# Kernel optimization log

Measured on AMD Instinct MI355X. Metric: run time of the kernel, lower is better.

## Reference

```python
import jax, jax.numpy as jnp
import numpy as np


def _spmm(rows, cols, vals, h, n):
    # sparse_dense_matmul(A, h) with A in COO form: out[r] += val * h[c]
    return jax.ops.segment_sum(vals[:, None] * h[cols], rows, num_segments=n)


def setup_inputs() -> dict:
    key = jax.random.key(0)
    ks = jax.random.split(key, 8)
    N, Din, Dout, D, E = 50000, 256, 128, 8, 800000
    x = jax.random.normal(ks[0], (N, Din), jnp.float32)
    h = jax.random.normal(ks[1], (N, Dout), jnp.float32)
    rows = jax.random.randint(ks[2], (D, E), 0, N, dtype=jnp.int32)
    cols = jax.random.randint(ks[3], (D, E), 0, N, dtype=jnp.int32)
    vals = jax.random.uniform(ks[4], (D, E), jnp.float32)
    W = jax.random.normal(ks[5], (Din, Dout), jnp.float32) * 0.05
    V = jax.random.normal(ks[6], (Dout, Dout), jnp.float32) * 0.05
    alpha = jax.random.normal(ks[7], (D, 1), jnp.float32)
    return dict(x=x, h=h, rows=rows, cols=cols, vals=vals, W=W, V=V, alpha=alpha)


def reference(x, h, rows, cols, vals, W, V, alpha):
    N = x.shape[0]
    D = rows.shape[0]
    # h1 = x @ W (x is tf.SparseTensor in the original; same math densely)
    h1 = x @ W
    # per-device: (A_d @ h) @ V  -> [D, N, Dout]; loop over small fixed device set
    h2 = jnp.stack([_spmm(rows[d], cols[d], vals[d], h, N) @ V for d in range(D)])
    # tf.nn.softmax on [D,1] normalizes the size-1 last axis -> all ones (faithful)
    w = jax.nn.softmax(alpha, axis=-1)[:, 0]  # [D]
    comb = jnp.einsum('dno,d->no', h2, w)  # matches reshape/transpose/matmul combine
    return jax.nn.relu(h1 + comb)
```

## Files before the change

kernel.cpp:

```cpp
#include <hip/hip_runtime.h>
#include <hip/hip_bf16.h>

#define DOUT 128
#define DIN  256
#define BROWS 64
#define MAXNB 1024
#define BIN_CHUNK 4096
#define SCHUNK 9216

typedef __attribute__((ext_vector_type(8))) short bf16x8;
typedef __attribute__((ext_vector_type(4))) float f32x4;
union FragU { uint4 q; bf16x8 f; };

static __device__ __forceinline__ float bf16lo_to_f(unsigned u) {
    return __uint_as_float(u << 16);
}
static __device__ __forceinline__ float bf16hi_to_f(unsigned u) {
    return __uint_as_float(u & 0xffff0000u);
}
static __device__ __forceinline__ unsigned f_to_bf16_bits(float f) {
    unsigned u = __float_as_uint(f);
    return (u + 0x7fffu + ((u >> 16) & 1u)) >> 16;
}
static __device__ __forceinline__ unsigned pack2(float a, float b) {
    return f_to_bf16_bits(a) | (f_to_bf16_bits(b) << 16);
}

__global__ __launch_bounds__(256) void conv_wv(const float* __restrict__ W,
                                               const float* __restrict__ V,
                                               unsigned short* __restrict__ WT,
                                               unsigned short* __restrict__ VT) {
    int n = blockIdx.x;
    int t = threadIdx.x;
    WT[n * 256 + t] = (unsigned short)f_to_bf16_bits(W[t * DOUT + n]);
    if (t < 128) VT[n * 128 + t] = (unsigned short)f_to_bf16_bits(V[t * DOUT + n]);
}

__global__ __launch_bounds__(256) void hv_gemm(const float* __restrict__ h,
                                               const unsigned* __restrict__ VTu,
                                               unsigned short* __restrict__ hV,
                                               int N) {
    __shared__ unsigned xs[64 * 20];
    int t = threadIdx.x;
    int r0 = blockIdx.x * 64;
    int w = t >> 6, l = t & 63;
    int wm = w >> 1, wn = w & 1;
    int lm = l & 15, lk = l >> 4;
    f32x4 acc[2][4];
#pragma unroll
    for (int i = 0; i < 2; ++i)
#pragma unroll
        for (int j = 0; j < 4; ++j) acc[i][j] = (f32x4){0.f, 0.f, 0.f, 0.f};

    int srow = min(r0 + (t >> 2), N - 1);
    const float* hrow = h + (size_t)srow * DOUT + (t & 3) * 8;
    unsigned* xsw = &xs[(t >> 2) * 20 + (t & 3) * 4];

    for (int k0 = 0; k0 < DOUT; k0 += 32) {
        float4 f0 = *(const float4*)(hrow + k0);
        float4 f1 = *(const float4*)(hrow + k0 + 4);
        ((uint4*)xsw)[0] = make_uint4(pack2(f0.x, f0.y), pack2(f0.z, f0.w),
                                      pack2(f1.x, f1.y), pack2(f1.z, f1.w));
        __syncthreads();
        FragU a[2], b[4];
#pragma unroll
        for (int i = 0; i < 2; ++i)
            a[i].q = *(const uint4*)&xs[(wm * 32 + i * 16 + lm) * 20 + lk * 4];
#pragma unroll
        for (int j = 0; j < 4; ++j)
            b[j].q = *(const uint4*)(VTu + (size_t)(wn * 64 + j * 16 + lm) * 64 +
                                     (k0 >> 1) + lk * 4);
#pragma unroll
        for (int i = 0; i < 2; ++i)
#pragma unroll
            for (int j = 0; j < 4; ++j)
                acc[i][j] = __builtin_amdgcn_mfma_f32_16x16x32_bf16(
                    a[i].f, b[j].f, acc[i][j], 0, 0, 0);
        __syncthreads();
    }
#pragma unroll
    for (int i = 0; i < 2; ++i)
#pragma unroll
        for (int j = 0; j < 4; ++j) {
            int gr0 = r0 + wm * 32 + i * 16 + lk * 4;
            int gc = wn * 64 + j * 16 + lm;
#pragma unroll
            for (int r = 0; r < 4; ++r) {
                int gr = gr0 + r;
                if (gr < N)
                    hV[(size_t)gr * DOUT + gc] =
                        (unsigned short)f_to_bf16_bits(acc[i][j][r]);
            }
        }
}

__global__ void bucket_hist(const int* __restrict__ rows, int* __restrict__ gcnt,
                            int nE, int nb) {
    __shared__ int hc[MAXNB];
    for (int i = threadIdx.x; i < nb; i += blockDim.x) hc[i] = 0;
    __syncthreads();
    for (int i = blockIdx.x * blockDim.x + threadIdx.x; i < nE;
         i += gridDim.x * blockDim.x)
        atomicAdd(&hc[rows[i] / BROWS], 1);
    __syncthreads();
    for (int i = threadIdx.x; i < nb; i += blockDim.x)
        if (hc[i]) atomicAdd(&gcnt[i], hc[i]);
}

__global__ __launch_bounds__(1024) void scan_buckets(const int* __restrict__ gcnt,
                                                     int* __restrict__ bptr,
                                                     int* __restrict__ gcur, int nb) {
    __shared__ int wtot[16];
    int t = threadIdx.x;
    int c = (t < nb) ? gcnt[t] : 0;
    int v = c;
#pragma unroll
    for (int d = 1; d < 64; d <<= 1) {
        int u = __shfl_up(v, d);
        if ((t & 63) >= d) v += u;
    }
    if ((t & 63) == 63) wtot[t >> 6] = v;
    __syncthreads();
    if (t < 16) {
        int wv = wtot[t];
#pragma unroll
        for (int d = 1; d < 16; d <<= 1) {
            int u = __shfl_up(wv, d);
            if (t >= d) wv += u;
        }
        wtot[t] = wv;
    }
    __syncthreads();
    int incl = v + ((t >= 64) ? wtot[(t >> 6) - 1] : 0);
    if (t == 0) bptr[0] = 0;
    if (t < nb) { bptr[t + 1] = incl; gcur[t] = incl - c; }
}

__global__ __launch_bounds__(1024) void bin_edges(const int* __restrict__ rows,
                                                  const int* __restrict__ cols,
                                                  const float* __restrict__ vals,
                                                  int* __restrict__ gcur,
                                                  unsigned* __restrict__ ecv4,
                                                  unsigned char* __restrict__ erow,
                                                  int nE, int nb) {
    __shared__ unsigned secv[BIN_CHUNK];
    __shared__ unsigned short srow16[BIN_CHUNK];
    __shared__ int hcnt[MAXNB], loff[MAXNB], lcur[MAXNB], gbase[MAXNB];
    __shared__ int wtot[16];
    int t = threadIdx.x;
    int base = blockIdx.x * BIN_CHUNK;
    int nvalid = min(BIN_CHUNK, nE - base);
    hcnt[t] = 0;
    __syncthreads();
    for (int j = t; j < nvalid; j += 1024)
        atomicAdd(&hcnt[rows[base + j] / BROWS], 1);
    __syncthreads();
    int myc = hcnt[t];
    int v = myc;
#pragma unroll
    for (int d = 1; d < 64; d <<= 1) {
        int u = __shfl_up(v, d);
        if ((t & 63) >= d) v += u;
    }
    if ((t & 63) == 63) wtot[t >> 6] = v;
    __syncthreads();
    if (t < 16) {
        int wv = wtot[t];
#pragma unroll
        for (int d = 1; d < 16; d <<= 1) {
            int u = __shfl_up(wv, d);
            if (t >= d) wv += u;
        }
        wtot[t] = wv;
    }
    __syncthreads();
    int excl = v - myc + ((t >= 64) ? wtot[(t >> 6) - 1] : 0);
    loff[t] = excl;
    lcur[t] = excl;
    if (t < nb && myc > 0) gbase[t] = atomicAdd(&gcur[t], myc);
    __syncthreads();
    for (int j = t; j < nvalid; j += 1024) {
        int i = base + j;
        unsigned r = (unsigned)rows[i];
        int bk = (int)r / BROWS;
        int slot = atomicAdd(&lcur[bk], 1);
        secv[slot] = ((unsigned)cols[i] << 16) | f_to_bf16_bits(vals[i]);
        srow16[slot] = (unsigned short)r;
    }
    __syncthreads();
    for (int j = t; j < nvalid; j += 1024) {
        unsigned r = srow16[j];
        int bk = (int)r / BROWS;
        int dst = gbase[bk] + (j - loff[bk]);
        ecv4[dst] = secv[j];
        erow[dst] = (unsigned char)(r & (BROWS - 1));
    }
}

__global__ __launch_bounds__(512) void spmm_epi(const int* __restrict__ bptr,
                                                const unsigned* __restrict__ ecv4,
                                                const unsigned char* __restrict__ erow,
                                                const unsigned* __restrict__ hV,
                                                const float* __restrict__ x,
                                                const unsigned* __restrict__ WTu,
                                                float* __restrict__ out, int N) {
    __shared__ __align__(16) unsigned srec[SCHUNK + BROWS * 8];
    __shared__ int rcnt[BROWS], rptr[BROWS + 1], rcur[BROWS];
    int t = threadIdx.x;
    int b = blockIdx.x;
    int wave = t >> 6, lane = t & 63;
    int hf = lane >> 5;
    int cl = lane & 31;
    int beg = bptr[b], end = bptr[b + 1];
    const uint2* hv2 = (const uint2*)hV;

    float4 acc[8];
#pragma unroll
    for (int j = 0; j < 8; ++j) acc[j] = make_float4(0.f, 0.f, 0.f, 0.f);

    for (int cb = beg; cb < end; cb += SCHUNK) {
        int nval = min(SCHUNK, end - cb);
        if (t < BROWS) rcnt[t] = 0;
        __syncthreads();
        for (int j = t; j < nval; j += 512)
            atomicAdd(&rcnt[erow[cb + j]], 1);
        __syncthreads();
        if (wave == 0) {
            int c = rcnt[lane];
            int cp = (c + 7) & ~7;
            int v = cp;
#pragma unroll
            for (int d = 1; d < 64; d <<= 1) {
                int u = __shfl_up(v, d);
                if (lane >= d) v += u;
            }
            rptr[lane + 1] = v;
            rcur[lane] = v - cp;
            if (lane == 0) rptr[0] = 0;
        }
        __syncthreads();
        for (int j = t; j < nval; j += 512) {
            int rloc = erow[cb + j];
            int slot = atomicAdd(&rcur[rloc], 1);
            srec[slot] = ecv4[cb + j];
        }
        __syncthreads();
        if (t < BROWS) {
            int e0 = rcur[t];
            int e1 = rptr[t + 1];
            for (int k = e0; k < e1; ++k) srec[k] = 0u;
        }
        __syncthreads();
#pragma unroll
        for (int rr = 0; rr < 8; ++rr) {
            int rloc = wave * 8 + rr;
            int s = rptr[rloc];
            int ng = (rptr[rloc + 1] - s) >> 3;
            const uint4* sp = (const uint4*)&srec[s + 4 * hf];
            float4 a = acc[rr];
            for (int g = 0; g < ng; ++g) {
                uint4 q = sp[2 * g];
                uint2 u0 = hv2[((q.x >> 16) << 5) | cl];
                uint2 u1 = hv2[((q.y >> 16) << 5) | cl];
                uint2 u2 = hv2[((q.z >> 16) << 5) | cl];
                uint2 u3 = hv2[((q.w >> 16) << 5) | cl];
                float v0 = bf16lo_to_f(q.x);
                float v1 = bf16lo_to_f(q.y);
                float v2 = bf16lo_to_f(q.z);
                float v3 = bf16lo_to_f(q.w);
                a.x += v0 * bf16lo_to_f(u0.x); a.y += v0 * bf16hi_to_f(u0.x);
                a.z += v0 * bf16lo_to_f(u0.y); a.w += v0 * bf16hi_to_f(u0.y);
                a.x += v1 * bf16lo_to_f(u1.x); a.y += v1 * bf16hi_to_f(u1.x);
                a.z += v1 * bf16lo_to_f(u1.y); a.w += v1 * bf16hi_to_f(u1.y);
                a.x += v2 * bf16lo_to_f(u2.x); a.y += v2 * bf16hi_to_f(u2.x);
                a.z += v2 * bf16lo_to_f(u2.y); a.w += v2 * bf16hi_to_f(u2.y);
                a.x += v3 * bf16lo_to_f(u3.x); a.y += v3 * bf16hi_to_f(u3.x);
                a.z += v3 * bf16lo_to_f(u3.y); a.w += v3 * bf16hi_to_f(u3.y);
            }
            acc[rr] = a;
        }
        __syncthreads();
    }

    float* Sbuf = (float*)srec;
#pragma unroll
    for (int rr = 0; rr < 8; ++rr) {
        float4 a = acc[rr];
        a.x += __shfl_xor(a.x, 32);
        a.y += __shfl_xor(a.y, 32);
        a.z += __shfl_xor(a.z, 32);
        a.w += __shfl_xor(a.w, 32);
        if (hf == 0)
            *(float4*)&Sbuf[(wave * 8 + rr) * 132 + 4 * cl] = a;
    }
    __syncthreads();

    unsigned* xs = srec + 64 * 132;
    int wm = wave >> 1, wn = wave & 1;
    int lm = lane & 15, lk = lane >> 4;
    f32x4 acc4[4];
#pragma unroll
    for (int j = 0; j < 4; ++j) acc4[j] = (f32x4){0.f, 0.f, 0.f, 0.f};

    int r0 = b * BROWS;
    int srow = min(r0 + (t >> 3), N - 1);
    const float* xrow = x + (size_t)srow * DIN + (t & 7) * 4;
    unsigned* xsw = &xs[(t >> 3) * 18 + (t & 7) * 2];

    for (int k0 = 0; k0 < DIN; k0 += 32) {
        float4 f = *(const float4*)(xrow + k0);
        xsw[0] = pack2(f.x, f.y);
        xsw[1] = pack2(f.z, f.w);
        __syncthreads();
        FragU a;
        a.q = *(const uint4*)&xs[(wm * 16 + lm) * 18 + lk * 4];
#pragma unroll
        for (int j = 0; j < 4; ++j) {
            FragU bb;
            bb.q = *(const uint4*)(WTu + (size_t)(wn * 64 + j * 16 + lm) * 128 +
                                   (k0 >> 1) + lk * 4);
            acc4[j] = __builtin_amdgcn_mfma_f32_16x16x32_bf16(
                a.f, bb.f, acc4[j], 0, 0, 0);
        }
        __syncthreads();
    }
#pragma unroll
    for (int j = 0; j < 4; ++j) {
        int gc = wn * 64 + j * 16 + lm;
#pragma unroll
        for (int r = 0; r < 4; ++r) {
            int lr = wm * 16 + 4 * lk + r;
            int gr = r0 + lr;
            if (gr < N)
                out[(size_t)gr * DOUT + gc] =
                    fmaxf(acc4[j][r] + Sbuf[lr * 132 + gc], 0.f);
        }
    }
}

__global__ void spmm_atomic(const int* __restrict__ rows,
                            const int* __restrict__ cols,
                            const float* __restrict__ vals,
                            const float* __restrict__ h,
                            float* __restrict__ S, int nEdges) {
    int wave = (int)((blockIdx.x * blockDim.x + threadIdx.x) >> 6);
    int lane = threadIdx.x & 63;
    if (wave >= nEdges) return;
    int r = rows[wave], c = cols[wave];
    float v = vals[wave];
    float2 hv = ((const float2*)(h + (size_t)c * DOUT))[lane];
    float* srow = S + (size_t)r * DOUT;
    atomicAdd(srow + 2 * lane,     v * hv.x);
    atomicAdd(srow + 2 * lane + 1, v * hv.y);
}

__global__ __launch_bounds__(256) void fused_out_full(const float* __restrict__ x,
                                                      const float* __restrict__ W,
                                                      const float* __restrict__ V,
                                                      float* __restrict__ out, int N) {
    __shared__ float xs[DIN];
    __shared__ float ss[DOUT];
    int r = blockIdx.x;
    int col = threadIdx.x & 127;
    if (threadIdx.x < 128) {
        float2 xv = ((const float2*)(x + (size_t)r * DIN))[col];
        xs[2 * col] = xv.x; xs[2 * col + 1] = xv.y;
        ss[col] = out[(size_t)r * DOUT + col];
    }
    __syncthreads();
    if (threadIdx.x >= 128) return;
    float acc = 0.f;
    for (int k = 0; k < DIN; ++k) acc += xs[k] * W[k * DOUT + col];
    for (int k = 0; k < DOUT; ++k) acc += ss[k] * V[k * DOUT + col];
    out[(size_t)r * DOUT + col] = fmaxf(acc, 0.f);
}

static inline size_t align256(size_t v) { return (v + 255) & ~(size_t)255; }

extern "C" void kernel_launch(void* const* d_in, const int* in_sizes, int n_in,
                              void* d_out, int out_size, void* d_ws, size_t ws_size,
                              hipStream_t stream) {
    const float* x    = (const float*)d_in[0];
    const float* h    = (const float*)d_in[1];
    const int*   rows = (const int*)d_in[2];
    const int*   cols = (const int*)d_in[3];
    const float* vals = (const float*)d_in[4];
    const float* W    = (const float*)d_in[5];
    const float* V    = (const float*)d_in[6];

    int nE = in_sizes[2];
    int N  = in_sizes[1] / DOUT;
    int nb = (N + BROWS - 1) / BROWS;
    float* out = (float*)d_out;

    size_t o_hV   = 0;
    size_t o_WT   = o_hV   + align256((size_t)N * DOUT * 2);
    size_t o_VT   = o_WT   + align256((size_t)128 * 256 * 2);
    size_t o_gcnt = o_VT   + align256((size_t)128 * 128 * 2);
    size_t o_bptr = o_gcnt + align256((size_t)nb * 4);
    size_t o_gcur = o_bptr + align256((size_t)(nb + 1) * 4);
    size_t o_ecv4 = o_gcur + align256((size_t)nb * 4);
    size_t o_erow = o_ecv4 + align256((size_t)nE * 4);
    size_t need   = o_erow + (size_t)nE;

    if (ws_size >= need && N < 65536 && nb <= MAXNB) {
        char* p = (char*)d_ws;
        unsigned short* hV = (unsigned short*)(p + o_hV);
        unsigned short* WT = (unsigned short*)(p + o_WT);
        unsigned short* VT = (unsigned short*)(p + o_VT);
        int*      gcnt = (int*)(p + o_gcnt);
        int*      bptr = (int*)(p + o_bptr);
        int*      gcur = (int*)(p + o_gcur);
        unsigned* ecv4 = (unsigned*)(p + o_ecv4);
        unsigned char* erow = (unsigned char*)(p + o_erow);

        conv_wv<<<128, 256, 0, stream>>>(W, V, WT, VT);
        hv_gemm<<<(N + 63) / 64, 256, 0, stream>>>(h, (const unsigned*)VT, hV, N);
        hipMemsetAsync(gcnt, 0, (size_t)nb * 4, stream);
        bucket_hist<<<1024, 256, 0, stream>>>(rows, gcnt, nE, nb);
        scan_buckets<<<1, 1024, 0, stream>>>(gcnt, bptr, gcur, nb);
        bin_edges<<<(nE + BIN_CHUNK - 1) / BIN_CHUNK, 1024, 0, stream>>>(
            rows, cols, vals, gcur, ecv4, erow, nE, nb);
        spmm_epi<<<nb, 512, 0, stream>>>(bptr, ecv4, erow, (const unsigned*)hV,
                                         x, (const unsigned*)WT, out, N);
    } else {
        hipMemsetAsync(out, 0, (size_t)N * DOUT * 4, stream);
        spmm_atomic<<<(nE + 3) / 4, 256, 0, stream>>>(rows, cols, vals, h, out, nE);
        fused_out_full<<<N, 128, 0, stream>>>(x, W, V, out, N);
    }
}
```

Baseline: 491.3 us.

## Sub-bin SpMM edges by column region to improve gather locality

Edges get a 2-bit column-region tag packed into the row byte, and the SpMM kernel sorts each chunk into 4x64 bins. It processes all rows for one column region before moving to the next, with a barrier between regions. The goal is for concurrently running blocks to gather from a smaller slice of hV, so more of it stays in L2. This adds more padding per bin (up to 7 zeroed slots times 256 bins), a wider scan and extra barriers.

```diff
diff --git a/kernel.cpp b/kernel.cpp
--- a/kernel.cpp
+++ b/kernel.cpp
@@ -7,6 +7,8 @@
 #define MAXNB 1024
 #define BIN_CHUNK 4096
 #define SCHUNK 9216
+#define NREG 4
+#define SBINS (NREG * BROWS)
 
 typedef __attribute__((ext_vector_type(8))) short bf16x8;
 typedef __attribute__((ext_vector_type(4))) float f32x4;
@@ -142,9 +144,10 @@
                                                   int* __restrict__ gcur,
                                                   unsigned* __restrict__ ecv4,
                                                   unsigned char* __restrict__ erow,
-                                                  int nE, int nb) {
+                                                  int nE, int nb, float regInv) {
     __shared__ unsigned secv[BIN_CHUNK];
     __shared__ unsigned short srow16[BIN_CHUNK];
+    __shared__ unsigned char sreg[BIN_CHUNK];
     __shared__ int hcnt[MAXNB], loff[MAXNB], lcur[MAXNB], gbase[MAXNB];
     __shared__ int wtot[16];
     int t = threadIdx.x;
@@ -182,10 +185,13 @@
     for (int j = t; j < nvalid; j += 1024) {
         int i = base + j;
         unsigned r = (unsigned)rows[i];
+        int col = cols[i];
         int bk = (int)r / BROWS;
+        int reg = min(NREG - 1, (int)((float)col * regInv));
         int slot = atomicAdd(&lcur[bk], 1);
-        secv[slot] = ((unsigned)cols[i] << 16) | f_to_bf16_bits(vals[i]);
+        secv[slot] = ((unsigned)col << 16) | f_to_bf16_bits(vals[i]);
         srow16[slot] = (unsigned short)r;
+        sreg[slot] = (unsigned char)reg;
     }
     __syncthreads();
     for (int j = t; j < nvalid; j += 1024) {
@@ -193,7 +199,7 @@
         int bk = (int)r / BROWS;
         int dst = gbase[bk] + (j - loff[bk]);
         ecv4[dst] = secv[j];
-        erow[dst] = (unsigned char)(r & (BROWS - 1));
+        erow[dst] = (unsigned char)((sreg[j] << 6) | (r & (BROWS - 1)));
     }
 }
 
@@ -204,8 +210,8 @@
                                                 const float* __restrict__ x,
                                                 const unsigned* __restrict__ WTu,
                                                 float* __restrict__ out, int N) {
-    __shared__ __align__(16) unsigned srec[SCHUNK + BROWS * 8];
-    __shared__ int rcnt[BROWS], rptr[BROWS + 1], rcur[BROWS];
+    __shared__ __align__(16) unsigned srec[SCHUNK + SBINS * 8];
+    __shared__ int rcnt[SBINS], rptr[SBINS + 1], rcur[SBINS];
     int t = threadIdx.x;
     int b = blockIdx.x;
     int wave = t >> 6, lane = t & 63;
@@ -220,66 +226,80 @@
 
     for (int cb = beg; cb < end; cb += SCHUNK) {
         int nval = min(SCHUNK, end - cb);
-        if (t < BROWS) rcnt[t] = 0;
+        if (t < SBINS) rcnt[t] = 0;
         __syncthreads();
         for (int j = t; j < nval; j += 512)
             atomicAdd(&rcnt[erow[cb + j]], 1);
         __syncthreads();
         if (wave == 0) {
-            int c = rcnt[lane];
-            int cp = (c + 7) & ~7;
-            int v = cp;
+            int b0 = 4 * lane;
+            int c0 = (rcnt[b0] + 7) & ~7;
+            int c1 = (rcnt[b0 + 1] + 7) & ~7;
+            int c2 = (rcnt[b0 + 2] + 7) & ~7;
+            int c3 = (rcnt[b0 + 3] + 7) & ~7;
+            int s1 = c0 + c1, s2 = s1 + c2, tot = s2 + c3;
+            int v = tot;
 #pragma unroll
             for (int d = 1; d < 64; d <<= 1) {
                 int u = __shfl_up(v, d);
                 if (lane >= d) v += u;
             }
-            rptr[lane + 1] = v;
-            rcur[lane] = v - cp;
+            int base0 = v - tot;
+            rptr[b0 + 1] = base0 + c0;
+            rptr[b0 + 2] = base0 + s1;
+            rptr[b0 + 3] = base0 + s2;
+            rptr[b0 + 4] = base0 + tot;
+            rcur[b0]     = base0;
+            rcur[b0 + 1] = base0 + c0;
+            rcur[b0 + 2] = base0 + s1;
+            rcur[b0 + 3] = base0 + s2;
             if (lane == 0) rptr[0] = 0;
         }
         __syncthreads();
         for (int j = t; j < nval; j += 512) {
-            int rloc = erow[cb + j];
-            int slot = atomicAdd(&rcur[rloc], 1);
+            int bin = erow[cb + j];
+            int slot = atomicAdd(&rcur[bin], 1);
             srec[slot] = ecv4[cb + j];
         }
         __syncthreads();
-        if (t < BROWS) {
+        if (t < SBINS) {
             int e0 = rcur[t];
             int e1 = rptr[t + 1];
             for (int k = e0; k < e1; ++k) srec[k] = 0u;
         }
         __syncthreads();
 #pragma unroll
-        for (int rr = 0; rr < 8; ++rr) {
-            int rloc = wave * 8 + rr;
-            int s = rptr[rloc];
-            int ng = (rptr[rloc + 1] - s) >> 3;
-            const uint4* sp = (const uint4*)&srec[s + 4 * hf];
-            float4 a = acc[rr];
-            for (int g = 0; g < ng; ++g) {
-                uint4 q = sp[2 * g];
-                uint2 u0 = hv2[((q.x >> 16) << 5) | cl];
-                uint2 u1 = hv2[((q.y >> 16) << 5) | cl];
-                uint2 u2 = hv2[((q.z >> 16) << 5) | cl];
-                uint2 u3 = hv2[((q.w >> 16) << 5) | cl];
-                float v0 = bf16lo_to_f(q.x);
-                float v1 = bf16lo_to_f(q.y);
-                float v2 = bf16lo_to_f(q.z);
-                float v3 = bf16lo_to_f(q.w);
-                a.x += v0 * bf16lo_to_f(u0.x); a.y += v0 * bf16hi_to_f(u0.x);
-                a.z += v0 * bf16lo_to_f(u0.y); a.w += v0 * bf16hi_to_f(u0.y);
-                a.x += v1 * bf16lo_to_f(u1.x); a.y += v1 * bf16hi_to_f(u1.x);
-                a.z += v1 * bf16lo_to_f(u1.y); a.w += v1 * bf16hi_to_f(u1.y);
-                a.x += v2 * bf16lo_to_f(u2.x); a.y += v2 * bf16hi_to_f(u2.x);
-                a.z += v2 * bf16lo_to_f(u2.y); a.w += v2 * bf16hi_to_f(u2.y);
-                a.x += v3 * bf16lo_to_f(u3.x); a.y += v3 * bf16hi_to_f(u3.x);
-                a.z += v3 * bf16lo_to_f(u3.y); a.w += v3 * bf16hi_to_f(u3.y);
+        for (int p = 0; p < NREG; ++p) {
+#pragma unroll
+            for (int rr = 0; rr < 8; ++rr) {
+                int bin = (p << 6) | (wave << 3) | rr;
+                int s = rptr[bin];
+                int ng = (rptr[bin + 1] - s) >> 3;
+                const uint4* sp = (const uint4*)&srec[s + 4 * hf];
+                float4 a = acc[rr];
+                for (int g = 0; g < ng; ++g) {
+                    uint4 q = sp[2 * g];
+                    uint2 u0 = hv2[((q.x >> 16) << 5) | cl];
+                    uint2 u1 = hv2[((q.y >> 16) << 5) | cl];
+                    uint2 u2 = hv2[((q.z >> 16) << 5) | cl];
+                    uint2 u3 = hv2[((q.w >> 16) << 5) | cl];
+                    float v0 = bf16lo_to_f(q.x);
+                    float v1 = bf16lo_to_f(q.y);
+                    float v2 = bf16lo_to_f(q.z);
+                    float v3 = bf16lo_to_f(q.w);
+                    a.x += v0 * bf16lo_to_f(u0.x); a.y += v0 * bf16hi_to_f(u0.x);
+                    a.z += v0 * bf16lo_to_f(u0.y); a.w += v0 * bf16hi_to_f(u0.y);
+                    a.x += v1 * bf16lo_to_f(u1.x); a.y += v1 * bf16hi_to_f(u1.x);
+                    a.z += v1 * bf16lo_to_f(u1.y); a.w += v1 * bf16hi_to_f(u1.y);
+                    a.x += v2 * bf16lo_to_f(u2.x); a.y += v2 * bf16hi_to_f(u2.x);
+                    a.z += v2 * bf16lo_to_f(u2.y); a.w += v2 * bf16hi_to_f(u2.y);
+                    a.x += v3 * bf16lo_to_f(u3.x); a.y += v3 * bf16hi_to_f(u3.x);
+                    a.z += v3 * bf16lo_to_f(u3.y); a.w += v3 * bf16hi_to_f(u3.y);
+                }
+                acc[rr] = a;
             }
-            acc[rr] = a;
-        }
-        __syncthreads();
+            __syncthreads();
+        }
     }
 
     float* Sbuf = (float*)srec;
@@ -392,6 +412,7 @@
     int N  = in_sizes[1] / DOUT;
     int nb = (N + BROWS - 1) / BROWS;
     float* out = (float*)d_out;
+    float regInv = (float)NREG / (float)N;
 
     size_t o_hV   = 0;
     size_t o_WT   = o_hV   + align256((size_t)N * DOUT * 2);
@@ -420,7 +441,7 @@
         bucket_hist<<<1024, 256, 0, stream>>>(rows, gcnt, nE, nb);
         scan_buckets<<<1, 1024, 0, stream>>>(gcnt, bptr, gcur, nb);
         bin_edges<<<(nE + BIN_CHUNK - 1) / BIN_CHUNK, 1024, 0, stream>>>(
-            rows, cols, vals, gcur, ecv4, erow, nE, nb);
+            rows, cols, vals, gcur, ecv4, erow, nE, nb, regInv);
         spmm_epi<<<nb, 512, 0, stream>>>(bptr, ecv4, erow, (const unsigned*)hV,
                                          x, (const unsigned*)WT, out, N);
     } else {
```

Result: faster. 472.4 us (-3.8%).
